# Kernel tuning notes

Measured on AMD Instinct MI355X. Metric: run time of the kernel, lower is better.

## Reference

```python
import jax, jax.numpy as jnp
import numpy as np

DIM = 256
STATE = 64
D_INNER = 256  # ssd_expand=1 * dim
HIDDEN = 1024  # mlp_ratio=4 * dim
EPS = 1e-5


def ln2d(x, w, b):
    # channel LayerNorm over dim 1 of [B,C,H,W]
    u = x.mean(1, keepdims=True)
    s = ((x - u) ** 2).mean(1, keepdims=True)
    return w[None, :, None, None] * ((x - u) * jax.lax.rsqrt(s + EPS)) + b[None, :, None, None]


def dwconv3x3(x, w, b=None):
    # depthwise 3x3, pad 1; x [B,C,H,W], w [C,1,3,3]
    y = jax.lax.conv_general_dilated(
        x, w, (1, 1), [(1, 1), (1, 1)],
        dimension_numbers=("NCHW", "OIHW", "NCHW"),
        feature_group_count=x.shape[1])
    if b is not None:
        y = y + b[None, :, None, None]
    return y


def setup_inputs() -> dict:
    key = jax.random.key(0)
    ks = jax.random.split(key, 20)
    rn = lambda k, shp, s=0.05: (s * jax.random.normal(k, shp)).astype(jnp.float32)
    inp = {
        "x": jax.random.normal(ks[0], (16, DIM, 64, 64), dtype=jnp.float32),
        "alpha": rn(ks[1], (4, DIM), 0.1),
        "ln_w": jnp.ones((DIM,)), "ln_b": jnp.zeros((DIM,)),
        "dw1_w": rn(ks[2], (DIM, 1, 3, 3), 0.1),
        "dw1_ln_w": jnp.ones((DIM,)), "dw1_ln_b": jnp.zeros((DIM,)),
        "dw2_w": rn(ks[3], (DIM, 1, 3, 3), 0.1),
        "dw2_ln_w": jnp.ones((DIM,)), "dw2_ln_b": jnp.zeros((DIM,)),
        "bcdt_w": rn(ks[4], (3 * STATE, DIM)),
        "bcdt_b": jnp.zeros((3 * STATE,)),
        "dwm_w": rn(ks[5], (3 * STATE, 1, 3, 3), 0.1),
        "dwm_b": jnp.zeros((3 * STATE,)),
        "hz_w": rn(ks[6], (2 * D_INNER, DIM)),
        "hz_b": jnp.zeros((2 * D_INNER,)),
        "outp_w": rn(ks[7], (DIM, D_INNER)),
        "outp_b": jnp.zeros((DIM,)),
        "A": jax.random.uniform(ks[8], (STATE,), minval=1.0, maxval=16.0).astype(jnp.float32),
        "Dp": jnp.ones((DIM,)),
        "fc1_w": rn(ks[9], (HIDDEN, DIM)),
        "fc1_ln_w": jnp.ones((HIDDEN,)), "fc1_ln_b": jnp.zeros((HIDDEN,)),
        "fc2_w": rn(ks[10], (DIM, HIDDEN)),
        "fc2_ln_w": jnp.ones((DIM,)), "fc2_ln_b": jnp.zeros((DIM,)),
    }
    return inp


def reference(x, alpha, ln_w, ln_b, dw1_w, dw1_ln_w, dw1_ln_b, dw2_w, dw2_ln_w, dw2_ln_b,
              bcdt_w, bcdt_b, dwm_w, dwm_b, hz_w, hz_b, outp_w, outp_b, A, Dp,
              fc1_w, fc1_ln_w, fc1_ln_b, fc2_w, fc2_ln_w, fc2_ln_b):
    a = jax.nn.sigmoid(alpha)[:, None, :, None, None]  # [4,1,dim,1,1]

    # sub-layer 1: depthwise conv + LN, gated residual
    x1 = (1.0 - a[0]) * x + a[0] * ln2d(dwconv3x3(x, dw1_w), dw1_ln_w, dw1_ln_b)

    # HSMSSD mixer on LayerNorm2D(x1)
    xn = ln2d(x1, ln_w, ln_b)
    Bb, Dd, H, W = xn.shape
    L = H * W
    xf = xn.reshape(Bb, Dd, L)
    bcdt = jnp.einsum("oc,bcl->bol", bcdt_w, xf) + bcdt_b[None, :, None]
    bcdt = dwconv3x3(bcdt.reshape(Bb, 3 * STATE, H, W), dwm_w, dwm_b).reshape(Bb, 3 * STATE, L)
    Bm, Cm, dt = jnp.split(bcdt, [STATE, 2 * STATE], axis=1)  # each [B,S,L]
    Asm = jax.nn.softmax(dt + A[None, :, None], axis=-1)
    AB = Asm * Bm
    h = jnp.einsum("bdl,bsl->bds", xf, AB)  # [B,D,S]
    hz = jnp.einsum("oc,bcs->bos", hz_w, h) + hz_b[None, :, None]
    hp, z = jnp.split(hz, [D_INNER], axis=1)
    hg = hp * jax.nn.silu(z)
    ho = jnp.einsum("oc,bcs->bos", outp_w, hg) + outp_b[None, :, None]
    y = jnp.einsum("bds,bsl->bdl", ho, Cm).reshape(Bb, Dd, H, W)
    y = y + xn * Dp[None, :, None, None]

    x2 = (1.0 - a[1]) * x1 + a[1] * y
    x3 = (1.0 - a[2]) * x2 + a[2] * ln2d(dwconv3x3(x2, dw2_w), dw2_ln_w, dw2_ln_b)

    # FFN: 1x1 conv -> LN -> SiLU -> 1x1 conv -> LN
    f1 = jax.nn.silu(ln2d(jnp.einsum("oc,bchw->bohw", fc1_w, x3), fc1_ln_w, fc1_ln_b))
    f2 = ln2d(jnp.einsum("oc,bchw->bohw", fc2_w, f1), fc2_ln_w, fc2_ln_b)
    x4 = (1.0 - a[3]) * x3 + a[3] * f2
    return (x4, h)
```

## Files before the change

### kernel.cpp

```cpp
#include <hip/hip_runtime.h>
#include <math.h>

#define LPOS 4096
#define NB 16

typedef __bf16 bf16;
typedef __bf16 bf16x8 __attribute__((ext_vector_type(8)));
typedef __bf16 bf16x4 __attribute__((ext_vector_type(4)));
typedef float f32x4 __attribute__((ext_vector_type(4)));

#define GLOAD_LDS16(g, l) \
    __builtin_amdgcn_global_load_lds((const __attribute__((address_space(1))) unsigned int*)(g), \
                                     (__attribute__((address_space(3))) unsigned int*)(l), 16, 0, 0)

#define SWZ512(byte) ((byte) ^ (((((unsigned)(byte)) >> 9) & 7) << 4))

__device__ __forceinline__ float sigm(float x){ return 1.f/(1.f+expf(-x)); }

__global__ void dwconv3x3_k(const float* __restrict__ in, const float* __restrict__ w9,
                            const float* __restrict__ bias, float* __restrict__ out, int C)
{
    int bc = blockIdx.x;
    int c = bc % C;
    __shared__ float tile[66][72];
    const float* p = in + (size_t)bc * LPOS;
    int tid = threadIdx.x;
    for (int i = tid; i < 144; i += 256) {
        int r = (i < 72) ? 0 : 65;
        int cc = i % 72;
        tile[r][cc] = 0.f;
    }
    if (tid < 64) { tile[tid+1][3] = 0.f; tile[tid+1][68] = 0.f; }
#pragma unroll
    for (int j = 0; j < 4; j++) {
        int f = tid + j*256;
        int y = f >> 4, x4 = (f & 15) << 2;
        *(f32x4*)&tile[1+y][4+x4] = *(const f32x4*)&p[y*64 + x4];
    }
    __syncthreads();
    float w[9];
#pragma unroll
    for (int i = 0; i < 9; i++) w[i] = w9[c*9 + i];
    float bb = bias ? bias[c] : 0.f;
    float* q = out + (size_t)bc * LPOS;
#pragma unroll
    for (int j = 0; j < 4; j++) {
        int f = tid + j*256;
        int y = f >> 4, x4 = (f & 15) << 2;
        f32x4 acc = {bb, bb, bb, bb};
#pragma unroll
        for (int dy = 0; dy < 3; dy++) {
            const float* row = &tile[y+dy][3 + x4];
            float t0 = row[0], t1 = row[1], t2 = row[2];
            float t3 = row[3], t4 = row[4], t5 = row[5];
            float w0 = w[dy*3], w1 = w[dy*3+1], w2 = w[dy*3+2];
            acc[0] += w0*t0 + w1*t1 + w2*t2;
            acc[1] += w0*t1 + w1*t2 + w2*t3;
            acc[2] += w0*t2 + w1*t3 + w2*t4;
            acc[3] += w0*t3 + w1*t4 + w2*t5;
        }
        *(f32x4*)&q[y*64 + x4] = acc;
    }
}

__global__ __launch_bounds__(512)
void ln_x1xn_k(const float* __restrict__ conv, const float* __restrict__ xin,
               float* __restrict__ x1, bf16* __restrict__ xnC, bf16* __restrict__ xnT,
               const float* __restrict__ dww, const float* __restrict__ dwb,
               const float* __restrict__ g0,
               const float* __restrict__ lnw, const float* __restrict__ lnb)
{
    int b = blockIdx.x >> 6;
    int tx = threadIdx.x;
    int ty = threadIdx.y;
    int p0 = ((blockIdx.x & 63) << 6) + (tx << 2);
    __shared__ float rs[32][68], rs2[32][68];
    int tid = ty*16 + tx;
    f32x4 vals[8];
    f32x4 s = {0.f,0.f,0.f,0.f}, s2 = {0.f,0.f,0.f,0.f};
    size_t bi = ((size_t)b*256 + ty*8)*LPOS + p0;
#pragma unroll
    for (int i = 0; i < 8; i++) {
        f32x4 x = *(const f32x4*)&conv[bi + (size_t)i*LPOS];
        vals[i] = x; s += x; s2 += x*x;
    }
#pragma unroll
    for (int q = 0; q < 4; q++) { rs[ty][tx*4+q] = s[q]; rs2[ty][tx*4+q] = s2[q]; }
    __syncthreads();
    {
        int r = tid >> 6, cc = tid & 63;
        rs[r][cc]  = rs[r][cc]  + rs[r+8][cc]  + rs[r+16][cc]  + rs[r+24][cc];
        rs2[r][cc] = rs2[r][cc] + rs2[r+8][cc] + rs2[r+16][cc] + rs2[r+24][cc];
    }
    __syncthreads();
    f32x4 S = {0.f,0.f,0.f,0.f}, S2 = {0.f,0.f,0.f,0.f};
#pragma unroll
    for (int j = 0; j < 8; j++) {
        S  += *(const f32x4*)&rs[j][tx*4];
        S2 += *(const f32x4*)&rs2[j][tx*4];
    }
    f32x4 u, inv;
#pragma unroll
    for (int q = 0; q < 4; q++) {
        float uu = S[q]*(1.f/256.f);
        u[q] = uu;
        inv[q] = rsqrtf(S2[q]*(1.f/256.f) - uu*uu + 1e-5f);
    }
    __syncthreads();
    s = (f32x4){0.f,0.f,0.f,0.f}; s2 = (f32x4){0.f,0.f,0.f,0.f};
#pragma unroll
    for (int i = 0; i < 8; i++) {
        int c = ty*8 + i;
        float w = dww[c], bbc = dwb[c];
        float g = sigm(g0[c]);
        f32x4 xv = *(const f32x4*)&xin[bi + (size_t)i*LPOS];
        f32x4 r;
#pragma unroll
        for (int q = 0; q < 4; q++) {
            float ln = w*((vals[i][q]-u[q])*inv[q]) + bbc;
            r[q] = (1.f-g)*xv[q] + g*ln;
        }
        vals[i] = r;
        *(f32x4*)&x1[bi + (size_t)i*LPOS] = r;
        s += r; s2 += r*r;
    }
#pragma unroll
    for (int q = 0; q < 4; q++) { rs[ty][tx*4+q] = s[q]; rs2[ty][tx*4+q] = s2[q]; }
    __syncthreads();
    {
        int r = tid >> 6, cc = tid & 63;
        rs[r][cc]  = rs[r][cc]  + rs[r+8][cc]  + rs[r+16][cc]  + rs[r+24][cc];
        rs2[r][cc] = rs2[r][cc] + rs2[r+8][cc] + rs2[r+16][cc] + rs2[r+24][cc];
    }
    __syncthreads();
    S = (f32x4){0.f,0.f,0.f,0.f}; S2 = (f32x4){0.f,0.f,0.f,0.f};
#pragma unroll
    for (int j = 0; j < 8; j++) {
        S  += *(const f32x4*)&rs[j][tx*4];
        S2 += *(const f32x4*)&rs2[j][tx*4];
    }
#pragma unroll
    for (int q = 0; q < 4; q++) {
        float uu = S[q]*(1.f/256.f);
        u[q] = uu;
        inv[q] = rsqrtf(S2[q]*(1.f/256.f) - uu*uu + 1e-5f);
    }
    bf16 tmp[32];
#pragma unroll
    for (int i = 0; i < 8; i++) {
        int c = ty*8 + i;
        float w = lnw[c], bbc = lnb[c];
        bf16x4 o;
#pragma unroll
        for (int q = 0; q < 4; q++) {
            float xnv = w*((vals[i][q]-u[q])*inv[q]) + bbc;
            o[q] = (bf16)xnv;
            tmp[q*8+i] = (bf16)xnv;
        }
        *(bf16x4*)&xnC[bi + (size_t)i*LPOS] = o;
    }
#pragma unroll
    for (int q = 0; q < 4; q++) {
        bf16x8* dst = (bf16x8*)&xnT[((size_t)b*LPOS + p0 + q)*256 + ty*8];
        *dst = *(bf16x8*)&tmp[q*8];
    }
}

__global__ __launch_bounds__(512)
void ln2d_k(const float* __restrict__ v, const float* __restrict__ base,
            float* __restrict__ out, const float* __restrict__ lnw,
            const float* __restrict__ lnb, const float* __restrict__ gate,
            bf16* __restrict__ auxT, int mode)
{
    int b = blockIdx.x >> 6;
    int tx = threadIdx.x;
    int ty = threadIdx.y;
    int p0 = ((blockIdx.x & 63) << 6) + (tx << 2);
    __shared__ float rs[32][68], rs2[32][68];
    int tid = ty*16 + tx;
    f32x4 vals[8];
    f32x4 s = {0.f,0.f,0.f,0.f}, s2 = {0.f,0.f,0.f,0.f};
    size_t bi = ((size_t)b*256 + ty*8)*LPOS + p0;
#pragma unroll
    for (int i = 0; i < 8; i++) {
        f32x4 x = *(const f32x4*)&v[bi + (size_t)i*LPOS];
        vals[i] = x; s += x; s2 += x*x;
    }
#pragma unroll
    for (int q = 0; q < 4; q++) { rs[ty][tx*4+q] = s[q]; rs2[ty][tx*4+q] = s2[q]; }
    __syncthreads();
    {
        int r = tid >> 6, cc = tid & 63;
        rs[r][cc]  = rs[r][cc]  + rs[r+8][cc]  + rs[r+16][cc]  + rs[r+24][cc];
        rs2[r][cc] = rs2[r][cc] + rs2[r+8][cc] + rs2[r+16][cc] + rs2[r+24][cc];
    }
    __syncthreads();
    f32x4 S = {0.f,0.f,0.f,0.f}, S2 = {0.f,0.f,0.f,0.f};
#pragma unroll
    for (int j = 0; j < 8; j++) {
        S  += *(const f32x4*)&rs[j][tx*4];
        S2 += *(const f32x4*)&rs2[j][tx*4];
    }
    f32x4 u, inv;
#pragma unroll
    for (int q = 0; q < 4; q++) {
        float uu = S[q]*(1.f/256.f);
        u[q] = uu;
        inv[q] = rsqrtf(S2[q]*(1.f/256.f) - uu*uu + 1e-5f);
    }
    bf16 tmp[32];
#pragma unroll
    for (int i = 0; i < 8; i++) {
        int c = ty*8 + i;
        float w = lnw[c], bbc = lnb[c];
        f32x4 r;
        if (mode == 0) {
#pragma unroll
            for (int q = 0; q < 4; q++) r[q] = w*((vals[i][q]-u[q])*inv[q]) + bbc;
        } else {
            float g = sigm(gate[c]);
            f32x4 bs = *(const f32x4*)&base[bi + (size_t)i*LPOS];
#pragma unroll
            for (int q = 0; q < 4; q++) {
                float ln = w*((vals[i][q]-u[q])*inv[q]) + bbc;
                r[q] = (1.f-g)*bs[q] + g*ln;
            }
        }
        *(f32x4*)&out[bi + (size_t)i*LPOS] = r;
#pragma unroll
        for (int q = 0; q < 4; q++) tmp[q*8+i] = (bf16)r[q];
    }
    if (auxT) {
#pragma unroll
        for (int q = 0; q < 4; q++) {
            bf16x8* dst = (bf16x8*)&auxT[((size_t)b*LPOS + p0 + q)*256 + ty*8];
            *dst = *(bf16x8*)&tmp[q*8];
        }
    }
}

__global__ void f2b_k(const float* __restrict__ in, bf16* __restrict__ out, int n)
{
    int i = blockIdx.x*256 + threadIdx.x;
    if (i < n) out[i] = (bf16)in[i];
}

__global__ void pad_w_k(const float* __restrict__ w, bf16* __restrict__ out)
{
    int i = blockIdx.x*256 + threadIdx.x;
    int r = i >> 8;
    out[i] = (r < 192) ? (bf16)w[(size_t)r*256 + (i & 255)] : (bf16)0.f;
}

__global__ void transpose_cm_k(const float* __restrict__ Cm, bf16* __restrict__ CmT)
{
    int b = blockIdx.y;
    int l0 = blockIdx.x * 64;
    const float* src = Cm + (size_t)b * 192 * LPOS;
    bf16* dst = CmT + (size_t)b * LPOS * 64;
    __shared__ float t[64][65];
    int tid = threadIdx.x;
    for (int i = tid; i < 4096; i += 256) {
        int s = i >> 6, l = i & 63;
        t[s][l] = src[(size_t)s*LPOS + l0 + l];
    }
    __syncthreads();
    for (int i = tid; i < 4096; i += 256) {
        int l = i >> 6, s = i & 63;
        dst[(size_t)(l0+l)*64 + s] = (bf16)t[s][l];
    }
}

__global__ void softmax_ab_k(const float* __restrict__ bcdt2, bf16* __restrict__ ABb,
                             const float* __restrict__ Avec)
{
    int b = blockIdx.x >> 6, s = blockIdx.x & 63;
    size_t base = (size_t)b*192*LPOS;
    const f32x4* dt = (const f32x4*)(bcdt2 + base + (size_t)(128+s)*LPOS);
    const f32x4* Bm = (const f32x4*)(bcdt2 + base + (size_t)s*LPOS);
    bf16* outp = ABb + ((size_t)b*64 + s)*LPOS;
    int tid = threadIdx.x;
    float av = Avec[s];
    f32x4 v[4];
    float mx = -1e30f;
#pragma unroll
    for (int i = 0; i < 4; i++) {
        f32x4 x = dt[tid + (i<<8)];
#pragma unroll
        for (int q = 0; q < 4; q++) { x[q] += av; mx = fmaxf(mx, x[q]); }
        v[i] = x;
    }
    __shared__ float red[256];
    red[tid] = mx; __syncthreads();
    for (int o = 128; o > 0; o >>= 1) {
        if (tid < o) red[tid] = fmaxf(red[tid], red[tid+o]);
        __syncthreads();
    }
    mx = red[0];
    __syncthreads();
    float sum = 0.f;
#pragma unroll
    for (int i = 0; i < 4; i++)
#pragma unroll
        for (int q = 0; q < 4; q++) { v[i][q] = expf(v[i][q]-mx); sum += v[i][q]; }
    red[tid] = sum; __syncthreads();
    for (int o = 128; o > 0; o >>= 1) {
        if (tid < o) red[tid] += red[tid+o];
        __syncthreads();
    }
    float rinv = 1.f / red[0];
#pragma unroll
    for (int i = 0; i < 4; i++) {
        f32x4 bm = Bm[tid + (i<<8)];
        bf16x4 o;
#pragma unroll
        for (int q = 0; q < 4; q++) o[q] = (bf16)(v[i][q] * rinv * bm[q]);
        ((bf16x4*)outp)[tid + (i<<8)] = o;
    }
}

__global__ __launch_bounds__(512)
void mixer_tail_k(const float* __restrict__ h, const float* __restrict__ hz_w,
                  const float* __restrict__ hz_b, const float* __restrict__ outp_w,
                  const float* __restrict__ outp_b, bf16* __restrict__ hob16)
{
    __shared__ bf16 hT[64*256];
    __shared__ bf16 hzs[512*64];
    int b = blockIdx.x;
    int tid = threadIdx.x;
    int lane = tid & 63, w = tid >> 6;
    int fm = lane & 15, quad = lane >> 4;

    const float* hb = h + (size_t)b*256*64;
#pragma unroll
    for (int j = 0; j < 8; j++) {
        int e4 = tid + j*512;
        f32x4 v = *(const f32x4*)&hb[e4*4];
        int k = (e4*4) >> 6;
        int n = (e4*4) & 63;
#pragma unroll
        for (int q = 0; q < 4; q++) {
            int byte = (n+q)*512 + k*2;
            *(bf16*)((char*)hT + SWZ512(byte)) = (bf16)v[q];
        }
    }
    __syncthreads();

    int mw = w*64;
    f32x4 acc[4][4] = {};
#pragma unroll
    for (int ks = 0; ks < 8; ks++) {
        int k0 = ks*32;
        bf16x8 af[4], bfr[4];
#pragma unroll
        for (int i = 0; i < 4; i++) {
            const float* wp = &hz_w[(size_t)(mw + i*16 + fm)*256 + k0 + quad*8];
            f32x4 w0 = *(const f32x4*)wp;
            f32x4 w1 = *(const f32x4*)(wp + 4);
#pragma unroll
            for (int q = 0; q < 4; q++) { af[i][q] = (bf16)w0[q]; af[i][4+q] = (bf16)w1[q]; }
        }
#pragma unroll
        for (int j = 0; j < 4; j++) {
            int n = j*16 + fm;
            int byte = n*512 + (k0 + quad*8)*2;
            bfr[j] = *(const bf16x8*)((const char*)hT + SWZ512(byte));
        }
#pragma unroll
        for (int i = 0; i < 4; i++)
#pragma unroll
            for (int j = 0; j < 4; j++)
                acc[i][j] = __builtin_amdgcn_mfma_f32_16x16x32_bf16(af[i], bfr[j], acc[i][j], 0, 0, 0);
    }
#pragma unroll
    for (int i = 0; i < 4; i++)
#pragma unroll
        for (int r = 0; r < 4; r++) {
            int m = mw + i*16 + quad*4 + r;
            float bb = hz_b[m];
#pragma unroll
            for (int j = 0; j < 4; j++)
                hzs[m*64 + j*16 + fm] = (bf16)(acc[i][j][r] + bb);
        }
    __syncthreads();

    {
        int k = tid >> 1, n0 = (tid & 1) * 32;
#pragma unroll
        for (int c = 0; c < 4; c++) {
            bf16x8 hp = *(const bf16x8*)&hzs[k*64 + n0 + c*8];
            bf16x8 zz = *(const bf16x8*)&hzs[(k+256)*64 + n0 + c*8];
#pragma unroll
            for (int q = 0; q < 8; q++) {
                float z = (float)zz[q];
                float g = (float)hp[q] * z * sigm(z);
                int byte = (n0 + c*8 + q)*512 + k*2;
                *(bf16*)((char*)hT + SWZ512(byte)) = (bf16)g;
            }
        }
    }
    __syncthreads();

    int mw2 = w*32;
    f32x4 acc2[2][4] = {};
#pragma unroll
    for (int ks = 0; ks < 8; ks++) {
        int k0 = ks*32;
        bf16x8 af[2], bfr[4];
#pragma unroll
        for (int i = 0; i < 2; i++) {
            const float* wp = &outp_w[(size_t)(mw2 + i*16 + fm)*256 + k0 + quad*8];
            f32x4 w0 = *(const f32x4*)wp;
            f32x4 w1 = *(const f32x4*)(wp + 4);
#pragma unroll
            for (int q = 0; q < 4; q++) { af[i][q] = (bf16)w0[q]; af[i][4+q] = (bf16)w1[q]; }
        }
#pragma unroll
        for (int j = 0; j < 4; j++) {
            int n = j*16 + fm;
            int byte = n*512 + (k0 + quad*8)*2;
            bfr[j] = *(const bf16x8*)((const char*)hT + SWZ512(byte));
        }
#pragma unroll
        for (int i = 0; i < 2; i++)
#pragma unroll
            for (int j = 0; j < 4; j++)
                acc2[i][j] = __builtin_amdgcn_mfma_f32_16x16x32_bf16(af[i], bfr[j], acc2[i][j], 0, 0, 0);
    }
    bf16* ob = hob16 + (size_t)b*256*64;
#pragma unroll
    for (int i = 0; i < 2; i++)
#pragma unroll
        for (int r = 0; r < 4; r++) {
            int m = mw2 + i*16 + quad*4 + r;
            float bb = outp_b[m];
#pragma unroll
            for (int j = 0; j < 4; j++)
                ob[m*64 + j*16 + fm] = (bf16)(acc2[i][j][r] + bb);
        }
}

template<int OUT_BF16>
__global__ __launch_bounds__(256)
void gemm_nt_mfma(const bf16* __restrict__ A, const bf16* __restrict__ B,
                  void* __restrict__ C, const float* __restrict__ bias, int mlimit,
                  int K, int lda, int ldb, int ldc,
                  size_t abst, size_t bbst, size_t cbst)
{
    int b = blockIdx.z;
    const bf16* Ab = A + (size_t)b*abst;
    const bf16* Bb = B + (size_t)b*bbst;
    int m0 = blockIdx.y*128, n0 = blockIdx.x*128;
    __shared__ bf16 Asl[128*64];
    __shared__ bf16 Bsl[128*64];
    int tid = threadIdx.x;
    int lane = tid & 63;
    int w = tid >> 6;
    int wm = (w >> 1)*64, wn = (w & 1)*64;
    int fm = lane & 15, quad = lane >> 4;
    f32x4 acc[4][4] = {};
    for (int k0 = 0; k0 < K; k0 += 64) {
#pragma unroll
        for (int ii = 0; ii < 4; ii++) {
            int q = ii*256 + tid;
            int row = q >> 3, ko = (q & 7) << 3;
            GLOAD_LDS16(Ab + (size_t)(m0+row)*lda + k0 + ko, &Asl[q*8]);
            GLOAD_LDS16(Bb + (size_t)(n0+row)*ldb + k0 + ko, &Bsl[q*8]);
        }
        __syncthreads();
#pragma unroll
        for (int kk = 0; kk < 2; kk++) {
            bf16x8 af[4], bfr[4];
#pragma unroll
            for (int i = 0; i < 4; i++)
                af[i] = *(const bf16x8*)&Asl[(wm + i*16 + fm)*64 + kk*32 + quad*8];
#pragma unroll
            for (int j = 0; j < 4; j++)
                bfr[j] = *(const bf16x8*)&Bsl[(wn + j*16 + fm)*64 + kk*32 + quad*8];
#pragma unroll
            for (int i = 0; i < 4; i++)
#pragma unroll
                for (int j = 0; j < 4; j++)
                    acc[i][j] = __builtin_amdgcn_mfma_f32_16x16x32_bf16(af[i], bfr[j], acc[i][j], 0, 0, 0);
        }
        __syncthreads();
    }
    size_t cb = (size_t)b*cbst;
#pragma unroll
    for (int i = 0; i < 4; i++) {
#pragma unroll
        for (int r = 0; r < 4; r++) {
            int m = m0 + wm + i*16 + quad*4 + r;
            if (m >= mlimit) continue;
            float bb = bias ? bias[m] : 0.f;
#pragma unroll
            for (int j = 0; j < 4; j++) {
                int n = n0 + wn + j*16 + fm;
                float vv = acc[i][j][r] + bb;
                if (OUT_BF16) ((bf16*)C)[cb + (size_t)m*ldc + n] = (bf16)vv;
                else          ((float*)C)[cb + (size_t)m*ldc + n] = vv;
            }
        }
    }
}

__global__ __launch_bounds__(256)
void gemm_h_mfma(const bf16* __restrict__ xnC, const bf16* __restrict__ ABb,
                 float* __restrict__ h, int Kchunk)
{
    int b = blockIdx.z;
    const bf16* Ab = xnC + (size_t)b*256*LPOS;
    const bf16* Bb = ABb + (size_t)b*64*LPOS;
    float* Cb = h + (size_t)b*256*64;
    int m0 = blockIdx.y*128;
    int kbase = blockIdx.x*Kchunk;
    __shared__ bf16 Asl[128*64];
    __shared__ bf16 Bsl[64*64];
    int tid = threadIdx.x;
    int lane = tid & 63;
    int w = tid >> 6;
    int wm = (w >> 1)*64, wn = (w & 1)*32;
    int fm = lane & 15, quad = lane >> 4;
    f32x4 acc[4][2] = {};
    for (int k0 = kbase; k0 < kbase + Kchunk; k0 += 64) {
#pragma unroll
        for (int ii = 0; ii < 4; ii++) {
            int q = ii*256 + tid;
            int row = q >> 3, ko = (q & 7) << 3;
            GLOAD_LDS16(Ab + (size_t)(m0+row)*LPOS + k0 + ko, &Asl[q*8]);
        }
#pragma unroll
        for (int ii = 0; ii < 2; ii++) {
            int q = ii*256 + tid;
            int row = q >> 3, ko = (q & 7) << 3;
            GLOAD_LDS16(Bb + (size_t)row*LPOS + k0 + ko, &Bsl[q*8]);
        }
        __syncthreads();
#pragma unroll
        for (int kk = 0; kk < 2; kk++) {
            bf16x8 af[4], bfr[2];
#pragma unroll
            for (int i = 0; i < 4; i++)
                af[i] = *(const bf16x8*)&Asl[(wm + i*16 + fm)*64 + kk*32 + quad*8];
#pragma unroll
            for (int j = 0; j < 2; j++)
                bfr[j] = *(const bf16x8*)&Bsl[(wn + j*16 + fm)*64 + kk*32 + quad*8];
#pragma unroll
            for (int i = 0; i < 4; i++)
#pragma unroll
                for (int j = 0; j < 2; j++)
                    acc[i][j] = __builtin_amdgcn_mfma_f32_16x16x32_bf16(af[i], bfr[j], acc[i][j], 0, 0, 0);
        }
        __syncthreads();
    }
#pragma unroll
    for (int i = 0; i < 4; i++)
#pragma unroll
        for (int r = 0; r < 4; r++) {
            int m = m0 + wm + i*16 + quad*4 + r;
#pragma unroll
            for (int j = 0; j < 2; j++) {
                int n = wn + j*16 + fm;
                atomicAdd(&Cb[(size_t)m*64 + n], acc[i][j][r]);
            }
        }
}

__global__ __launch_bounds__(256)
void mixer_out_mfma(const bf16* __restrict__ hoB, const bf16* __restrict__ CmT,
                    const bf16* __restrict__ xnC, float* __restrict__ x,
                    const float* __restrict__ Dp, const float* __restrict__ gate)
{
    int b = blockIdx.z;
    const bf16* Ab = hoB + (size_t)b*(256*64);
    const bf16* Bb = CmT + (size_t)b*((size_t)LPOS*64);
    int m0 = blockIdx.y*128, n0 = blockIdx.x*128;
    __shared__ bf16 Asl[128*64];
    __shared__ bf16 Bsl[128*64];
    int tid = threadIdx.x;
    int lane = tid & 63;
    int w = tid >> 6;
    int wm = (w >> 1)*64, wn = (w & 1)*64;
    int fm = lane & 15, quad = lane >> 4;
    f32x4 acc[4][4] = {};
#pragma unroll
    for (int ii = 0; ii < 4; ii++) {
        int q = ii*256 + tid;
        int row = q >> 3, ko = (q & 7) << 3;
        GLOAD_LDS16(Ab + (size_t)(m0+row)*64 + ko, &Asl[q*8]);
        GLOAD_LDS16(Bb + (size_t)(n0+row)*64 + ko, &Bsl[q*8]);
    }
    __syncthreads();
#pragma unroll
    for (int kk = 0; kk < 2; kk++) {
        bf16x8 af[4], bfr[4];
#pragma unroll
        for (int i = 0; i < 4; i++)
            af[i] = *(const bf16x8*)&Asl[(wm + i*16 + fm)*64 + kk*32 + quad*8];
#pragma unroll
        for (int j = 0; j < 4; j++)
            bfr[j] = *(const bf16x8*)&Bsl[(wn + j*16 + fm)*64 + kk*32 + quad*8];
#pragma unroll
        for (int i = 0; i < 4; i++)
#pragma unroll
            for (int j = 0; j < 4; j++)
                acc[i][j] = __builtin_amdgcn_mfma_f32_16x16x32_bf16(af[i], bfr[j], acc[i][j], 0, 0, 0);
    }
#pragma unroll
    for (int i = 0; i < 4; i++) {
#pragma unroll
        for (int r = 0; r < 4; r++) {
            int m = m0 + wm + i*16 + quad*4 + r;
            float g = sigm(gate[m]);
            float dp = Dp[m];
#pragma unroll
            for (int j = 0; j < 4; j++) {
                int n = n0 + wn + j*16 + fm;
                size_t idx = ((size_t)b*256 + m)*LPOS + n;
                float y = acc[i][j][r] + (float)xnC[idx]*dp;
                x[idx] = (1.f-g)*x[idx] + g*y;
            }
        }
    }
}

__global__ void ln_silu_rows_k(bf16* __restrict__ f, const float* __restrict__ w,
                               const float* __restrict__ bvec)
{
    size_t row = (size_t)blockIdx.x*4 + (threadIdx.x >> 6);
    int lane = threadIdx.x & 63;
    bf16* p = f + row*1024 + lane*16;
    bf16x8 v0 = *(const bf16x8*)p;
    bf16x8 v1 = *(const bf16x8*)(p + 8);
    float v[16];
    float s = 0.f, s2 = 0.f;
#pragma unroll
    for (int i = 0; i < 8; i++) { v[i] = (float)v0[i]; v[8+i] = (float)v1[i]; }
#pragma unroll
    for (int i = 0; i < 16; i++) { s += v[i]; s2 += v[i]*v[i]; }
    for (int o = 32; o > 0; o >>= 1) { s += __shfl_xor(s, o); s2 += __shfl_xor(s2, o); }
    float u = s * (1.f/1024.f);
    float var = s2 * (1.f/1024.f) - u*u;
    float inv = rsqrtf(var + 1e-5f);
#pragma unroll
    for (int i = 0; i < 16; i++) {
        int c = lane*16 + i;
        float ln = w[c]*((v[i]-u)*inv) + bvec[c];
        v[i] = ln * sigm(ln);
    }
    bf16x8 o0, o1;
#pragma unroll
    for (int i = 0; i < 8; i++) { o0[i] = (bf16)v[i]; o1[i] = (bf16)v[8+i]; }
    *(bf16x8*)p = o0;
    *(bf16x8*)(p + 8) = o1;
}

extern "C" void kernel_launch(void* const* d_in, const int* in_sizes, int n_in,
                              void* d_out, int out_size, void* d_ws, size_t ws_size,
                              hipStream_t stream)
{
    const float* x        = (const float*)d_in[0];
    const float* alpha    = (const float*)d_in[1];
    const float* ln_w     = (const float*)d_in[2];
    const float* ln_b     = (const float*)d_in[3];
    const float* dw1_w    = (const float*)d_in[4];
    const float* dw1_ln_w = (const float*)d_in[5];
    const float* dw1_ln_b = (const float*)d_in[6];
    const float* dw2_w    = (const float*)d_in[7];
    const float* dw2_ln_w = (const float*)d_in[8];
    const float* dw2_ln_b = (const float*)d_in[9];
    const float* bcdt_w   = (const float*)d_in[10];
    const float* bcdt_b   = (const float*)d_in[11];
    const float* dwm_w    = (const float*)d_in[12];
    const float* dwm_b    = (const float*)d_in[13];
    const float* hz_w     = (const float*)d_in[14];
    const float* hz_b     = (const float*)d_in[15];
    const float* outp_w   = (const float*)d_in[16];
    const float* outp_b   = (const float*)d_in[17];
    const float* Avec     = (const float*)d_in[18];
    const float* Dp       = (const float*)d_in[19];
    const float* fc1_w    = (const float*)d_in[20];
    const float* fc1_ln_w = (const float*)d_in[21];
    const float* fc1_ln_b = (const float*)d_in[22];
    const float* fc2_w    = (const float*)d_in[23];
    const float* fc2_ln_w = (const float*)d_in[24];
    const float* fc2_ln_b = (const float*)d_in[25];

    float* outp  = (float*)d_out;
    float* h_out = outp + (size_t)NB*256*LPOS;

    float* ws   = (float*)d_ws;
    float* bufA = ws;
    float* bufB = bufA + (size_t)NB*256*LPOS;
    float* bufC = bufB + (size_t)NB*256*LPOS;
    float* bufD = bufC + (size_t)NB*256*LPOS;
    float* hzb  = bufD + (size_t)NB*192*LPOS;

    bf16* CmT     = (bf16*)bufA;
    bf16* ABb     = (bf16*)(bufA + 8*1024*1024);
    float* f2buf  = bufA;
    bf16* xnC     = (bf16*)bufC;
    bf16* xnT     = xnC + (size_t)NB*256*LPOS;
    bf16* f1buf   = (bf16*)bufC;
    bf16* x3t     = (bf16*)bufD;
    bf16* fc1_wb  = (bf16*)(bufD + 9000000);
    bf16* fc2_wb  = (bf16*)(bufD + 9200000);
    bf16* hob16   = (bf16*)(bufD + 9400000);
    bf16* wpad    = (bf16*)hzb;

    dim3 blk256(256);
    dim3 blkLN(16, 32);

    dwconv3x3_k<<<dim3(NB*256), blk256, 0, stream>>>(x, dw1_w, nullptr, bufA, 256);
    ln_x1xn_k<<<dim3(NB*64), blkLN, 0, stream>>>(bufA, x, bufB, xnC, xnT,
                                                 dw1_ln_w, dw1_ln_b, alpha + 0, ln_w, ln_b);
    pad_w_k<<<dim3(256), blk256, 0, stream>>>(bcdt_w, wpad);
    gemm_nt_mfma<0><<<dim3(32, 2, NB), blk256, 0, stream>>>(
        wpad, xnT, (void*)bufA, bcdt_b, 192, 256, 256, 256, LPOS,
        0, (size_t)LPOS*256, (size_t)192*LPOS);
    dwconv3x3_k<<<dim3(NB*192), blk256, 0, stream>>>(bufA, dwm_w, dwm_b, bufD, 192);
    transpose_cm_k<<<dim3(64, NB), blk256, 0, stream>>>(bufD + (size_t)64*LPOS, CmT);
    softmax_ab_k<<<dim3(NB*64), blk256, 0, stream>>>(bufD, ABb, Avec);
    hipMemsetAsync(h_out, 0, (size_t)NB*256*64*sizeof(float), stream);
    gemm_h_mfma<<<dim3(4, 2, NB), blk256, 0, stream>>>(xnC, ABb, h_out, 1024);
    mixer_tail_k<<<dim3(NB), dim3(512), 0, stream>>>(h_out, hz_w, hz_b, outp_w, outp_b, hob16);
    f2b_k<<<dim3(1024), blk256, 0, stream>>>(fc1_w, fc1_wb, 1024*256);
    f2b_k<<<dim3(1024), blk256, 0, stream>>>(fc2_w, fc2_wb, 256*1024);
    mixer_out_mfma<<<dim3(32, 2, NB), blk256, 0, stream>>>(hob16, CmT, xnC, bufB, Dp, alpha + 256);
    dwconv3x3_k<<<dim3(NB*256), blk256, 0, stream>>>(bufB, dw2_w, nullptr, bufA, 256);
    ln2d_k<<<dim3(NB*64), blkLN, 0, stream>>>(bufA, bufB, bufB, dw2_ln_w, dw2_ln_b, alpha + 512, x3t, 1);
    for (int ch = 0; ch < 4; ch++) {
        const bf16*  x3tc = x3t + (size_t)ch*4*LPOS*256;
        const float* x3c  = bufB + (size_t)ch*4*256*LPOS;
        float* outc = outp + (size_t)ch*4*256*LPOS;
        gemm_nt_mfma<1><<<dim3(8, 32, 4), blk256, 0, stream>>>(
            x3tc, fc1_wb, (void*)f1buf, nullptr, 1<<30, 256, 256, 256, 1024,
            (size_t)LPOS*256, 0, (size_t)LPOS*1024);
        ln_silu_rows_k<<<dim3(4*LPOS/4), blk256, 0, stream>>>(f1buf, fc1_ln_w, fc1_ln_b);
        gemm_nt_mfma<0><<<dim3(32, 2, 4), blk256, 0, stream>>>(
            fc2_wb, f1buf, (void*)f2buf, nullptr, 1<<30, 1024, 1024, 1024, LPOS,
            0, (size_t)LPOS*1024, (size_t)256*LPOS);
        ln2d_k<<<dim3(4*64), blkLN, 0, stream>>>(f2buf, x3c, outc, fc2_ln_w, fc2_ln_b, alpha + 768, nullptr, 1);
    }
}
```

Measured before the change: 762.2 us.

## Fuse FC1 LayerNorm+SiLU into GEMM epilogue stats and FC2 prologue

New measurement: 904.4 us. 1.19x slower.

```diff
diff --git a/kernel.cpp b/kernel.cpp
--- a/kernel.cpp
+++ b/kernel.cpp
@@ -499,6 +499,159 @@
                 float vv = acc[i][j][r] + bb;
                 if (OUT_BF16) ((bf16*)C)[cb + (size_t)m*ldc + n] = (bf16)vv;
                 else          ((float*)C)[cb + (size_t)m*ldc + n] = vv;
+            }
+        }
+    }
+}
+
+__global__ __launch_bounds__(256)
+void gemm_fc1_stats(const bf16* __restrict__ A, const bf16* __restrict__ B,
+                    bf16* __restrict__ C, float* __restrict__ stats)
+{
+    int z = blockIdx.z;
+    const bf16* Ab = A + (size_t)z*LPOS*256;
+    bf16* Cb = C + (size_t)z*LPOS*1024;
+    int m0 = blockIdx.y*128, n0 = blockIdx.x*128;
+    __shared__ bf16 Asl[128*64];
+    __shared__ bf16 Bsl[128*64];
+    int tid = threadIdx.x;
+    int lane = tid & 63;
+    int w = tid >> 6;
+    int wm = (w >> 1)*64, wn = (w & 1)*64;
+    int fm = lane & 15, quad = lane >> 4;
+    f32x4 acc[4][4] = {};
+    for (int k0 = 0; k0 < 256; k0 += 64) {
+#pragma unroll
+        for (int ii = 0; ii < 4; ii++) {
+            int q = ii*256 + tid;
+            int row = q >> 3, ko = (q & 7) << 3;
+            GLOAD_LDS16(Ab + (size_t)(m0+row)*256 + k0 + ko, &Asl[q*8]);
+            GLOAD_LDS16(B + (size_t)(n0+row)*256 + k0 + ko, &Bsl[q*8]);
+        }
+        __syncthreads();
+#pragma unroll
+        for (int kk = 0; kk < 2; kk++) {
+            bf16x8 af[4], bfr[4];
+#pragma unroll
+            for (int i = 0; i < 4; i++)
+                af[i] = *(const bf16x8*)&Asl[(wm + i*16 + fm)*64 + kk*32 + quad*8];
+#pragma unroll
+            for (int j = 0; j < 4; j++)
+                bfr[j] = *(const bf16x8*)&Bsl[(wn + j*16 + fm)*64 + kk*32 + quad*8];
+#pragma unroll
+            for (int i = 0; i < 4; i++)
+#pragma unroll
+                for (int j = 0; j < 4; j++)
+                    acc[i][j] = __builtin_amdgcn_mfma_f32_16x16x32_bf16(af[i], bfr[j], acc[i][j], 0, 0, 0);
+        }
+        __syncthreads();
+    }
+#pragma unroll
+    for (int i = 0; i < 4; i++) {
+#pragma unroll
+        for (int r = 0; r < 4; r++) {
+            int m = m0 + wm + i*16 + quad*4 + r;
+            float s = 0.f, s2 = 0.f;
+#pragma unroll
+            for (int j = 0; j < 4; j++) {
+                int n = n0 + wn + j*16 + fm;
+                float vv = acc[i][j][r];
+                Cb[(size_t)m*1024 + n] = (bf16)vv;
+                s += vv; s2 += vv*vv;
+            }
+#pragma unroll
+            for (int msk = 1; msk <= 8; msk <<= 1) {
+                s  += __shfl_xor(s, msk);
+                s2 += __shfl_xor(s2, msk);
+            }
+            if (fm == 0) {
+                atomicAdd(&stats[(size_t)(z*LPOS + m)*2 + 0], s);
+                atomicAdd(&stats[(size_t)(z*LPOS + m)*2 + 1], s2);
+            }
+        }
+    }
+}
+
+__global__ __launch_bounds__(256)
+void gemm_fc2_fused(const bf16* __restrict__ A, const bf16* __restrict__ f1,
+                    const float* __restrict__ stats,
+                    const float* __restrict__ lw, const float* __restrict__ lb,
+                    float* __restrict__ Cout)
+{
+    int z = blockIdx.z;
+    const bf16* Bb = f1 + (size_t)z*LPOS*1024;
+    float* Cb = Cout + (size_t)z*256*LPOS;
+    int m0 = blockIdx.y*128, n0 = blockIdx.x*128;
+    __shared__ bf16 Asl[128*64];
+    __shared__ bf16 Bsl[128*64];
+    __shared__ float wsl[1024], bsl[1024];
+    int tid = threadIdx.x;
+    int lane = tid & 63;
+    int w = tid >> 6;
+    int wm = (w >> 1)*64, wn = (w & 1)*64;
+    int fm = lane & 15, quad = lane >> 4;
+    for (int i = tid; i < 1024; i += 256) { wsl[i] = lw[i]; bsl[i] = lb[i]; }
+    float us[4], iv[4];
+#pragma unroll
+    for (int ii = 0; ii < 4; ii++) {
+        int row = (ii*256 + tid) >> 3;
+        float sA = stats[(size_t)(z*LPOS + n0 + row)*2 + 0];
+        float sQ = stats[(size_t)(z*LPOS + n0 + row)*2 + 1];
+        float u = sA*(1.f/1024.f);
+        us[ii] = u;
+        iv[ii] = rsqrtf(sQ*(1.f/1024.f) - u*u + 1e-5f);
+    }
+    f32x4 acc[4][4] = {};
+    for (int k0 = 0; k0 < 1024; k0 += 64) {
+#pragma unroll
+        for (int ii = 0; ii < 4; ii++) {
+            int q = ii*256 + tid;
+            int row = q >> 3, ko = (q & 7) << 3;
+            GLOAD_LDS16(A + (size_t)(m0+row)*1024 + k0 + ko, &Asl[q*8]);
+        }
+#pragma unroll
+        for (int ii = 0; ii < 4; ii++) {
+            int q = ii*256 + tid;
+            int row = q >> 3, ko = (q & 7) << 3;
+            bf16x8 v = *(const bf16x8*)&Bb[(size_t)(n0+row)*1024 + k0 + ko];
+            float u = us[ii], inv = iv[ii];
+            bf16x8 o;
+#pragma unroll
+            for (int e = 0; e < 8; e++) {
+                int k = k0 + ko + e;
+                float x = ((float)v[e] - u)*inv;
+                x = wsl[k]*x + bsl[k];
+                o[e] = (bf16)(x*sigm(x));
+            }
+            *(bf16x8*)&Bsl[q*8] = o;
+        }
+        __syncthreads();
+#pragma unroll
+        for (int kk = 0; kk < 2; kk++) {
+            bf16x8 af[4], bfr[4];
+#pragma unroll
+            for (int i = 0; i < 4; i++)
+                af[i] = *(const bf16x8*)&Asl[(wm + i*16 + fm)*64 + kk*32 + quad*8];
+#pragma unroll
+            for (int j = 0; j < 4; j++)
+                bfr[j] = *(const bf16x8*)&Bsl[(wn + j*16 + fm)*64 + kk*32 + quad*8];
+#pragma unroll
+            for (int i = 0; i < 4; i++)
+#pragma unroll
+                for (int j = 0; j < 4; j++)
+                    acc[i][j] = __builtin_amdgcn_mfma_f32_16x16x32_bf16(af[i], bfr[j], acc[i][j], 0, 0, 0);
+        }
+        __syncthreads();
+    }
+#pragma unroll
+    for (int i = 0; i < 4; i++) {
+#pragma unroll
+        for (int r = 0; r < 4; r++) {
+            int m = m0 + wm + i*16 + quad*4 + r;
+#pragma unroll
+            for (int j = 0; j < 4; j++) {
+                int n = n0 + wn + j*16 + fm;
+                Cb[(size_t)m*LPOS + n] = acc[i][j][r];
             }
         }
     }
@@ -622,37 +775,6 @@
             }
         }
     }
-}
-
-__global__ void ln_silu_rows_k(bf16* __restrict__ f, const float* __restrict__ w,
-                               const float* __restrict__ bvec)
-{
-    size_t row = (size_t)blockIdx.x*4 + (threadIdx.x >> 6);
-    int lane = threadIdx.x & 63;
-    bf16* p = f + row*1024 + lane*16;
-    bf16x8 v0 = *(const bf16x8*)p;
-    bf16x8 v1 = *(const bf16x8*)(p + 8);
-    float v[16];
-    float s = 0.f, s2 = 0.f;
-#pragma unroll
-    for (int i = 0; i < 8; i++) { v[i] = (float)v0[i]; v[8+i] = (float)v1[i]; }
-#pragma unroll
-    for (int i = 0; i < 16; i++) { s += v[i]; s2 += v[i]*v[i]; }
-    for (int o = 32; o > 0; o >>= 1) { s += __shfl_xor(s, o); s2 += __shfl_xor(s2, o); }
-    float u = s * (1.f/1024.f);
-    float var = s2 * (1.f/1024.f) - u*u;
-    float inv = rsqrtf(var + 1e-5f);
-#pragma unroll
-    for (int i = 0; i < 16; i++) {
-        int c = lane*16 + i;
-        float ln = w[c]*((v[i]-u)*inv) + bvec[c];
-        v[i] = ln * sigm(ln);
-    }
-    bf16x8 o0, o1;
-#pragma unroll
-    for (int i = 0; i < 8; i++) { o0[i] = (bf16)v[i]; o1[i] = (bf16)v[8+i]; }
-    *(bf16x8*)p = o0;
-    *(bf16x8*)(p + 8) = o1;
 }
 
 extern "C" void kernel_launch(void* const* d_in, const int* in_sizes, int n_in,
@@ -706,6 +828,7 @@
     bf16* fc1_wb  = (bf16*)(bufD + 9000000);
     bf16* fc2_wb  = (bf16*)(bufD + 9200000);
     bf16* hob16   = (bf16*)(bufD + 9400000);
+    float* stats  = bufD + 10000000;
     bf16* wpad    = (bf16*)hzb;
 
     dim3 blk256(256);
@@ -733,13 +856,10 @@
         const bf16*  x3tc = x3t + (size_t)ch*4*LPOS*256;
         const float* x3c  = bufB + (size_t)ch*4*256*LPOS;
         float* outc = outp + (size_t)ch*4*256*LPOS;
-        gemm_nt_mfma<1><<<dim3(8, 32, 4), blk256, 0, stream>>>(
-            x3tc, fc1_wb, (void*)f1buf, nullptr, 1<<30, 256, 256, 256, 1024,
-            (size_t)LPOS*256, 0, (size_t)LPOS*1024);
-        ln_silu_rows_k<<<dim3(4*LPOS/4), blk256, 0, stream>>>(f1buf, fc1_ln_w, fc1_ln_b);
-        gemm_nt_mfma<0><<<dim3(32, 2, 4), blk256, 0, stream>>>(
-            fc2_wb, f1buf, (void*)f2buf, nullptr, 1<<30, 1024, 1024, 1024, LPOS,
-            0, (size_t)LPOS*1024, (size_t)256*LPOS);
+        hipMemsetAsync(stats, 0, (size_t)4*LPOS*2*sizeof(float), stream);
+        gemm_fc1_stats<<<dim3(8, 32, 4), blk256, 0, stream>>>(x3tc, fc1_wb, f1buf, stats);
+        gemm_fc2_fused<<<dim3(32, 2, 4), blk256, 0, stream>>>(fc2_wb, f1buf, stats,
+                                                              fc1_ln_w, fc1_ln_b, f2buf);
         ln2d_k<<<dim3(4*64), blkLN, 0, stream>>>(f2buf, x3c, outc, fc2_ln_w, fc2_ln_b, alpha + 768, nullptr, 1);
     }
 }
```

## Fuse fc2 GEMM with channel LayerNorm and gated residual epilogue

Applied to the files above, without the earlier changes.

Measured after the change: 761.5 us. About the same (-0.1%).

```diff
diff --git a/kernel.cpp b/kernel.cpp
--- a/kernel.cpp
+++ b/kernel.cpp
@@ -499,6 +499,101 @@
                 float vv = acc[i][j][r] + bb;
                 if (OUT_BF16) ((bf16*)C)[cb + (size_t)m*ldc + n] = (bf16)vv;
                 else          ((float*)C)[cb + (size_t)m*ldc + n] = vv;
+            }
+        }
+    }
+}
+
+__global__ __launch_bounds__(512)
+void gemm_fc2_out(const bf16* __restrict__ A, const bf16* __restrict__ f1,
+                  const float* __restrict__ x3, float* __restrict__ outp,
+                  const float* __restrict__ lw, const float* __restrict__ lb,
+                  const float* __restrict__ gate)
+{
+    int z = blockIdx.z;
+    const bf16* Bb = f1 + (size_t)z*LPOS*1024;
+    const float* x3b = x3 + (size_t)z*256*LPOS;
+    float* ob = outp + (size_t)z*256*LPOS;
+    int n0 = blockIdx.x*128;
+    __shared__ bf16 Asl[256*64];
+    __shared__ bf16 Bsl[128*64];
+    __shared__ float ps[4][128], ps2[4][128];
+    int tid = threadIdx.x;
+    int lane = tid & 63;
+    int w = tid >> 6;
+    int wm = (w >> 1)*64, wn = (w & 1)*64;
+    int fm = lane & 15, quad = lane >> 4;
+    f32x4 acc[4][4] = {};
+    for (int k0 = 0; k0 < 1024; k0 += 64) {
+#pragma unroll
+        for (int ii = 0; ii < 4; ii++) {
+            int q = ii*512 + tid;
+            int row = q >> 3, ko = (q & 7) << 3;
+            GLOAD_LDS16(A + (size_t)row*1024 + k0 + ko, &Asl[q*8]);
+        }
+#pragma unroll
+        for (int ii = 0; ii < 2; ii++) {
+            int q = ii*512 + tid;
+            int row = q >> 3, ko = (q & 7) << 3;
+            GLOAD_LDS16(Bb + (size_t)(n0+row)*1024 + k0 + ko, &Bsl[q*8]);
+        }
+        __syncthreads();
+#pragma unroll
+        for (int kk = 0; kk < 2; kk++) {
+            bf16x8 af[4], bfr[4];
+#pragma unroll
+            for (int i = 0; i < 4; i++)
+                af[i] = *(const bf16x8*)&Asl[(wm + i*16 + fm)*64 + kk*32 + quad*8];
+#pragma unroll
+            for (int j = 0; j < 4; j++)
+                bfr[j] = *(const bf16x8*)&Bsl[(wn + j*16 + fm)*64 + kk*32 + quad*8];
+#pragma unroll
+            for (int i = 0; i < 4; i++)
+#pragma unroll
+                for (int j = 0; j < 4; j++)
+                    acc[i][j] = __builtin_amdgcn_mfma_f32_16x16x32_bf16(af[i], bfr[j], acc[i][j], 0, 0, 0);
+        }
+        __syncthreads();
+    }
+#pragma unroll
+    for (int j = 0; j < 4; j++) {
+        float s = 0.f, s2 = 0.f;
+#pragma unroll
+        for (int i = 0; i < 4; i++)
+#pragma unroll
+            for (int r = 0; r < 4; r++) { float v = acc[i][j][r]; s += v; s2 += v*v; }
+        s  += __shfl_xor(s, 16);  s2 += __shfl_xor(s2, 16);
+        s  += __shfl_xor(s, 32);  s2 += __shfl_xor(s2, 32);
+        if (quad == 0) {
+            int n = wn + j*16 + fm;
+            ps[w >> 1][n] = s;
+            ps2[w >> 1][n] = s2;
+        }
+    }
+    __syncthreads();
+    float us[4], iv[4];
+#pragma unroll
+    for (int j = 0; j < 4; j++) {
+        int n = wn + j*16 + fm;
+        float S  = ps[0][n] + ps[1][n] + ps[2][n] + ps[3][n];
+        float S2 = ps2[0][n] + ps2[1][n] + ps2[2][n] + ps2[3][n];
+        float u = S*(1.f/256.f);
+        us[j] = u;
+        iv[j] = rsqrtf(S2*(1.f/256.f) - u*u + 1e-5f);
+    }
+#pragma unroll
+    for (int i = 0; i < 4; i++) {
+#pragma unroll
+        for (int r = 0; r < 4; r++) {
+            int m = wm + i*16 + quad*4 + r;
+            float g = sigm(gate[m]);
+            float lwm = lw[m], lbm = lb[m];
+#pragma unroll
+            for (int j = 0; j < 4; j++) {
+                int n = n0 + wn + j*16 + fm;
+                size_t idx = (size_t)m*LPOS + n;
+                float ln = lwm*((acc[i][j][r]-us[j])*iv[j]) + lbm;
+                ob[idx] = (1.f-g)*x3b[idx] + g*ln;
             }
         }
     }
@@ -698,7 +793,6 @@
 
     bf16* CmT     = (bf16*)bufA;
     bf16* ABb     = (bf16*)(bufA + 8*1024*1024);
-    float* f2buf  = bufA;
     bf16* xnC     = (bf16*)bufC;
     bf16* xnT     = xnC + (size_t)NB*256*LPOS;
     bf16* f1buf   = (bf16*)bufC;
@@ -737,9 +831,7 @@
             x3tc, fc1_wb, (void*)f1buf, nullptr, 1<<30, 256, 256, 256, 1024,
             (size_t)LPOS*256, 0, (size_t)LPOS*1024);
         ln_silu_rows_k<<<dim3(4*LPOS/4), blk256, 0, stream>>>(f1buf, fc1_ln_w, fc1_ln_b);
-        gemm_nt_mfma<0><<<dim3(32, 2, 4), blk256, 0, stream>>>(
-            fc2_wb, f1buf, (void*)f2buf, nullptr, 1<<30, 1024, 1024, 1024, LPOS,
-            0, (size_t)LPOS*1024, (size_t)256*LPOS);
-        ln2d_k<<<dim3(4*64), blkLN, 0, stream>>>(f2buf, x3c, outc, fc2_ln_w, fc2_ln_b, alpha + 768, nullptr, 1);
-    }
-}
+        gemm_fc2_out<<<dim3(32, 1, 4), dim3(512), 0, stream>>>(
+            fc2_wb, f1buf, x3c, outc, fc2_ln_w, fc2_ln_b, alpha + 768);
+    }
+}
```
